# Performance work log

Measured on AMD Instinct MI355X. Metric: run time of the kernel, lower is better.

## Reference

```python
import jax, jax.numpy as jnp
import numpy as np

VOCAB, NUM_CLASSES, C, H = 50257, 1000, 32, 512
B, T = 64, 1024
DECAY = 0.85


def setup_inputs() -> dict:
    key = jax.random.key(0)
    ks = jax.random.split(key, 16)
    s = 0.02
    return {
        "tokens": jax.random.randint(ks[0], (B, T), 0, VOCAB, dtype=jnp.int32),
        "emb": jax.random.normal(ks[1], (VOCAB, H), jnp.float32) * s,
        "w_ih": jax.random.normal(ks[2], (3 * H, H), jnp.float32) * s,
        "w_hh": jax.random.normal(ks[3], (3 * H, H), jnp.float32) * s,
        "b_ih": jax.random.normal(ks[4], (3 * H,), jnp.float32) * s,
        "b_hh": jax.random.normal(ks[5], (3 * H,), jnp.float32) * s,
        "wc": jax.random.normal(ks[6], (C * H, H), jnp.float32) * s,
        "bc": jax.random.normal(ks[7], (C * H,), jnp.float32) * s,
        "ws": jax.random.normal(ks[8], (C, H), jnp.float32) * s,
        "bs": jax.random.normal(ks[9], (C,), jnp.float32) * s,
        "ww": jax.random.normal(ks[10], (C, H), jnp.float32) * s,
        "bw": jax.random.normal(ks[11], (C,), jnp.float32) * s,
        "wcls": jax.random.normal(ks[12], (NUM_CLASSES, C * (H + 2)), jnp.float32) * s,
        "bcls": jax.random.normal(ks[13], (NUM_CLASSES,), jnp.float32) * s,
    }


def _gru(x, w_ih, w_hh, b_ih, b_hh):
    # x: [B,T,H]; torch GRU gate order: r, z, n
    xp = jnp.einsum('bth,gh->btg', x, w_ih) + b_ih          # [B,T,3H], batched GEMM
    xp = jnp.transpose(xp, (1, 0, 2))                        # [T,B,3H]

    def step(h, xp_t):
        hp = h @ w_hh.T + b_hh                               # [B,3H]
        xr, xz, xn = jnp.split(xp_t, 3, axis=-1)
        hr, hz, hn = jnp.split(hp, 3, axis=-1)
        r = jax.nn.sigmoid(xr + hr)
        z = jax.nn.sigmoid(xz + hz)
        n = jnp.tanh(xn + r * hn)
        h_new = (1.0 - z) * n + z * h
        return h_new, h_new

    h0 = jnp.zeros((x.shape[0], w_hh.shape[1]), x.dtype)
    _, h_seq = jax.lax.scan(step, h0, xp)                    # [T,B,H]
    return h_seq


def reference(tokens, emb, w_ih, w_hh, b_ih, b_hh, wc, bc, ws, bs, ww, bw, wcls, bcls):
    x = emb[tokens]                                          # [B,T,H]
    h_seq = _gru(x, w_ih, w_hh, b_ih, b_hh)                  # [T,B,H]
    Tn = h_seq.shape[0]

    # EMA with constant decay d: state_T = d^T*init + (1-d) * sum_t d^(T-1-t) * delta_t
    decay = DECAY ** (Tn - 1 - jnp.arange(Tn, dtype=jnp.float32))  # [T]

    # centers (linear delta, init 0): project the decay-weighted hidden sum once.
    hw = jnp.einsum('t,tbh->bh', decay, h_seq)               # [B,H]
    centers = (1 - DECAY) * (hw @ wc.T + decay.sum() * bc)   # [B,C*H]
    centers = centers.reshape(-1, C, H)                      # [B,C,H]

    # spreads (sigmoid delta, init 1)
    sd = jax.nn.sigmoid(jnp.einsum('tbh,ch->tbc', h_seq, ws) + bs)  # [T,B,C]
    spreads = DECAY ** Tn + (1 - DECAY) * jnp.einsum('t,tbc->bc', decay, sd)

    # weights (plain additive accumulation)
    weights = h_seq.sum(axis=0) @ ww.T + Tn * bw             # [B,C]
    nw = jax.nn.softmax(weights, axis=-1)

    summary = jnp.concatenate(
        [centers, spreads[..., None], nw[..., None]], axis=-1)  # [B,C,H+2]
    flat = summary.reshape(summary.shape[0], -1)
    return flat @ wcls.T + bcls
```

## Files before the change

### kernel.cpp

```cpp
#include <hip/hip_runtime.h>
#include <stddef.h>


typedef unsigned short u16;
typedef short s8v __attribute__((ext_vector_type(8)));
typedef float f4v __attribute__((ext_vector_type(4)));

#define B_ 64
#define T_ 1024
#define H_ 512
#define G_ 1536
#define C_ 32
#define NCLS_ 1000
#define KCLS_ 16448

#define AGENT __HIP_MEMORY_SCOPE_AGENT

__device__ __forceinline__ u16 f2bf(float f) {
    unsigned u = __float_as_uint(f);
    unsigned r = (u + 0x7fffu + ((u >> 16) & 1u)) >> 16;
    return (u16)r;
}
__device__ __forceinline__ float b2f(u16 x) { return __uint_as_float(((unsigned)x) << 16); }
__device__ __forceinline__ float bflo(unsigned u) { return __uint_as_float(u << 16); }
__device__ __forceinline__ float bfhi(unsigned u) { return __uint_as_float(u & 0xffff0000u); }
__device__ __forceinline__ float sigmoidf_(float x) { return 1.0f / (1.0f + __expf(-x)); }
__device__ __forceinline__ float tanhf_(float x) { return 1.0f - 2.0f / (1.0f + __expf(2.0f * x)); }

__global__ void k_cast_wih(const float* __restrict__ src, u16* __restrict__ dst) {
    int i = blockIdx.x * 256 + threadIdx.x;
    if (i < G_ * H_) dst[i] = f2bf(src[i]);
}

__global__ void k_pack_whhN(const float* __restrict__ w_hh, uint4* __restrict__ wN) {
    int idx = blockIdx.x * 256 + threadIdx.x;
    if (idx >= 4 * 64 * 384) return;
    int g = idx % 384;
    int k8 = (idx / 384) % 64;
    int s = idx / (384 * 64);
    int j = (g >> 7) * 512 + s * 128 + (g & 127);
    const float* wr = w_hh + (size_t)j * H_ + 8 * k8;
    uint4 v;
    v.x = (unsigned)f2bf(wr[0]) | ((unsigned)f2bf(wr[1]) << 16);
    v.y = (unsigned)f2bf(wr[2]) | ((unsigned)f2bf(wr[3]) << 16);
    v.z = (unsigned)f2bf(wr[4]) | ((unsigned)f2bf(wr[5]) << 16);
    v.w = (unsigned)f2bf(wr[6]) | ((unsigned)f2bf(wr[7]) << 16);
    wN[idx] = v;
}

__global__ void k_decay(float* __restrict__ decay) {
    int t = blockIdx.x * 256 + threadIdx.x;
    if (t < T_) decay[t] = powf(0.85f, (float)(T_ - 1 - t));
}

__global__ void k_zero(float* __restrict__ p, int n) {
    int i = blockIdx.x * 256 + threadIdx.x;
    if (i < n) p[i] = 0.f;
}

__global__ __launch_bounds__(256) void k_embed(const int* __restrict__ tokens,
                                               const float* __restrict__ emb,
                                               u16* __restrict__ X) {
    int g = blockIdx.x * 256 + threadIdx.x;
    int m = g >> 6, c8 = g & 63;
    int tok = tokens[m];
    const float4* src = (const float4*)(emb + (size_t)tok * H_ + c8 * 8);
    float4 f0 = src[0], f1 = src[1];
    uint4 pk;
    pk.x = (unsigned)f2bf(f0.x) | ((unsigned)f2bf(f0.y) << 16);
    pk.y = (unsigned)f2bf(f0.z) | ((unsigned)f2bf(f0.w) << 16);
    pk.z = (unsigned)f2bf(f1.x) | ((unsigned)f2bf(f1.y) << 16);
    pk.w = (unsigned)f2bf(f1.z) | ((unsigned)f2bf(f1.w) << 16);
    *(uint4*)(X + (size_t)m * H_ + c8 * 8) = pk;
}

__global__ __launch_bounds__(256) void k_xp(const u16* __restrict__ X,
                                            const u16* __restrict__ Wih,
                                            const float* __restrict__ b_ih,
                                            u16* __restrict__ xp) {
    __shared__ u16 Bs[128 * 48];
    int tid = threadIdx.x;
    int bid = blockIdx.x;
    int m0 = (bid / 12) * 64;
    int n0 = (bid % 12) * 128;
    int w = tid >> 6, lane = tid & 63;
    int lm = lane & 15, q = lane >> 4;
    f4v acc[8];
#pragma unroll
    for (int i = 0; i < 8; i++) acc[i] = (f4v){0.f, 0.f, 0.f, 0.f};
    int arow = m0 + w * 16 + lm;
    const u16* Aptr = X + (size_t)arow * H_ + q * 8;
    int srow = tid >> 1, shalf = tid & 1;
    for (int kk = 0; kk < H_; kk += 32) {
        const uint4* src = (const uint4*)(Wih + (size_t)(n0 + srow) * H_ + kk + shalf * 16);
        uint4 v0 = src[0], v1 = src[1];
        uint4* dst = (uint4*)(Bs + srow * 48 + shalf * 16);
        dst[0] = v0; dst[1] = v1;
        __syncthreads();
        s8v a = *(const s8v*)(Aptr + kk);
#pragma unroll
        for (int nt = 0; nt < 8; nt++) {
            s8v bf = *(const s8v*)(Bs + (nt * 16 + lm) * 48 + q * 8);
            acc[nt] = __builtin_amdgcn_mfma_f32_16x16x32_bf16(a, bf, acc[nt], 0, 0, 0);
        }
        __syncthreads();
    }
#pragma unroll
    for (int nt = 0; nt < 8; nt++) {
        int col = n0 + nt * 16 + lm;
        float bias = b_ih[col];
#pragma unroll
        for (int r = 0; r < 4; r++) {
            int row = m0 + w * 16 + q * 4 + r;
            xp[(size_t)row * G_ + col] = f2bf(acc[nt][r] + bias);
        }
    }
}

__global__ __launch_bounds__(512, 2) void k_scan4(const uint4* __restrict__ wN,
                                                  const u16* __restrict__ xp,
                                                  const float* __restrict__ b_hh,
                                                  float* __restrict__ hseq,
                                                  float* __restrict__ hx,
                                                  unsigned* __restrict__ flags) {
    int x = blockIdx.x;
    int s = x & 3, b = x >> 2;
    int tid = threadIdx.x;
    __shared__ float hl[2][512];
    __shared__ float dotb[3][128];
    hl[0][tid] = 0.f;
    const uint4* wS = wN + (size_t)s * (64 * 384);
    int io = tid & 127;
    int jo = s * 128 + io;
    float bh = 0.f;
    if (tid < 384) bh = b_hh[(tid >> 7) * H_ + jo];
    float hprev = 0.f;
    const u16* xpb = xp + (size_t)b * T_ * G_;
    unsigned* flg = flags + b * 64;
    __syncthreads();
    for (int t = 0; t < T_; t++) {
        int par = t & 1;
        float xr = 0.f, xz = 0.f, xn = 0.f;
        if (tid < 128) {
            const u16* xt = xpb + (size_t)t * G_;
            xr = b2f(xt[jo]); xz = b2f(xt[512 + jo]); xn = b2f(xt[1024 + jo]);
        }
        float acc = 0.f;
        if (tid < 384) {
            const float4* h4 = (const float4*)&hl[par][s * 128];
            const uint4* wp = wS + (size_t)(16 * s) * 384 + tid;
#pragma unroll
            for (int kk = 0; kk < 16; kk++) {
                uint4 wv = wp[(size_t)kk * 384];
                float4 ha = h4[2 * kk], hb = h4[2 * kk + 1];
                acc = fmaf(bflo(wv.x), ha.x, acc); acc = fmaf(bfhi(wv.x), ha.y, acc);
                acc = fmaf(bflo(wv.y), ha.z, acc); acc = fmaf(bfhi(wv.y), ha.w, acc);
                acc = fmaf(bflo(wv.z), hb.x, acc); acc = fmaf(bfhi(wv.z), hb.y, acc);
                acc = fmaf(bflo(wv.w), hb.z, acc); acc = fmaf(bfhi(wv.w), hb.w, acc);
            }
        } else if (t > 0) {
            int p = tid - 384;
            const float* hr = hx + ((size_t)par * B_ + b) * 512;
#pragma unroll
            for (int d = 1; d < 4; d++) {
                int s2 = (s + d) & 3;
                const unsigned* fl = flg + s2 * 16;
                while (__hip_atomic_load(fl, __ATOMIC_RELAXED, AGENT) < (unsigned)t)
                    __builtin_amdgcn_s_sleep(1);
                __asm__ __volatile__("" ::: "memory");
                hl[par][s2 * 128 + p] =
                    __hip_atomic_load(hr + s2 * 128 + p, __ATOMIC_RELAXED, AGENT);
            }
        }
        __syncthreads();
        if (tid < 384) {
#pragma unroll
            for (int d = 1; d < 4; d++) {
                int s2 = (s + d) & 3;
                const float4* h4 = (const float4*)&hl[par][s2 * 128];
                const uint4* wp = wS + (size_t)(16 * s2) * 384 + tid;
#pragma unroll
                for (int kk = 0; kk < 16; kk++) {
                    uint4 wv = wp[(size_t)kk * 384];
                    float4 ha = h4[2 * kk], hb = h4[2 * kk + 1];
                    acc = fmaf(bflo(wv.x), ha.x, acc); acc = fmaf(bfhi(wv.x), ha.y, acc);
                    acc = fmaf(bflo(wv.y), ha.z, acc); acc = fmaf(bfhi(wv.y), ha.w, acc);
                    acc = fmaf(bflo(wv.z), hb.x, acc); acc = fmaf(bfhi(wv.z), hb.y, acc);
                    acc = fmaf(bflo(wv.w), hb.z, acc); acc = fmaf(bfhi(wv.w), hb.w, acc);
                }
            }
            dotb[tid >> 7][io] = acc + bh;
        }
        __syncthreads();
        if (tid < 128) {
            float r = sigmoidf_(xr + dotb[0][io]);
            float z = sigmoidf_(xz + dotb[1][io]);
            float n = tanhf_(xn + r * dotb[2][io]);
            float hn = (1.f - z) * n + z * hprev;
            hprev = hn;
            hl[par ^ 1][jo] = hn;
            __hip_atomic_store(hx + ((size_t)(par ^ 1) * B_ + b) * 512 + jo, hn,
                               __ATOMIC_RELAXED, AGENT);
            hseq[((size_t)t * B_ + b) * H_ + jo] = hn;
        }
        __syncthreads();
        if (tid == 0)
            __hip_atomic_store(flg + s * 16, (unsigned)(t + 1), __ATOMIC_RELAXED, AGENT);
    }
}

__global__ __launch_bounds__(512) void k_hw8(const float* __restrict__ hseq,
                                             const float* __restrict__ decay,
                                             float* __restrict__ hwT,
                                             float* __restrict__ hsumT) {
    int b = blockIdx.x & 63, chunk = blockIdx.x >> 6;
    int h = threadIdx.x;
    int t0 = chunk * 128;
    float aw = 0.f, as = 0.f;
    for (int tt = 0; tt < 128; tt++) {
        float v = hseq[((size_t)(t0 + tt) * B_ + b) * H_ + h];
        aw = fmaf(decay[t0 + tt], v, aw);
        as += v;
    }
    atomicAdd(&hwT[h * B_ + b], aw);
    atomicAdd(&hsumT[h * B_ + b], as);
}

__global__ __launch_bounds__(512) void k_sd8(const float* __restrict__ hseq,
                                             const float* __restrict__ ws,
                                             const float* __restrict__ bs,
                                             const float* __restrict__ decay,
                                             float* __restrict__ flatT) {
    int b = blockIdx.x & 63, chunk = blockIdx.x >> 6;
    int t0 = chunk * 128;
    int tid = threadIdx.x;
    __shared__ float hl[2][512];
    int c = tid >> 4, p = tid & 15;
    float wreg[32];
#pragma unroll
    for (int i = 0; i < 32; i++) wreg[i] = ws[c * H_ + p + 16 * i];
    float bsc = bs[c];
    float acc = 0.f;
    hl[0][tid] = hseq[((size_t)t0 * B_ + b) * H_ + tid];
    __syncthreads();
    for (int tt = 0; tt < 128; tt++) {
        float nxt = 0.f;
        if (tt < 127) nxt = hseq[((size_t)(t0 + tt + 1) * B_ + b) * H_ + tid];
        int pg = tt & 1;
        float partial = 0.f;
#pragma unroll
        for (int i = 0; i < 32; i++) partial = fmaf(wreg[i], hl[pg][p + 16 * i], partial);
        partial += __shfl_xor(partial, 1, 16);
        partial += __shfl_xor(partial, 2, 16);
        partial += __shfl_xor(partial, 4, 16);
        partial += __shfl_xor(partial, 8, 16);
        acc = fmaf(decay[t0 + tt], sigmoidf_(partial + bsc), acc);
        __syncthreads();
        hl[pg ^ 1][tid] = nxt;
        __syncthreads();
    }
    if (p == 0) atomicAdd(&flatT[(c * 514 + 512) * B_ + b], 0.15f * acc);
}

__global__ __launch_bounds__(1024) void k_weights(const float* __restrict__ hsumT,
                                                  const float* __restrict__ ww,
                                                  const float* __restrict__ bw,
                                                  float* __restrict__ flatT) {
    int tid = threadIdx.x;
    __shared__ float wmat[C_ * B_];
    __shared__ float mb[B_], sb[B_];
    int b = tid & 63;
    int c0 = tid >> 6;
    float a0 = 0.f, a1 = 0.f;
    for (int h = 0; h < H_; h++) {
        float hv = hsumT[h * B_ + b];
        a0 = fmaf(ww[c0 * H_ + h], hv, a0);
        a1 = fmaf(ww[(c0 + 16) * H_ + h], hv, a1);
    }
    wmat[c0 * B_ + b] = a0 + 1024.0f * bw[c0];
    wmat[(c0 + 16) * B_ + b] = a1 + 1024.0f * bw[c0 + 16];
    __syncthreads();
    if (tid < 64) {
        float m = -1e30f;
        for (int c = 0; c < C_; c++) m = fmaxf(m, wmat[c * B_ + tid]);
        float sum = 0.f;
        for (int c = 0; c < C_; c++) sum += __expf(wmat[c * B_ + tid] - m);
        mb[tid] = m;
        sb[tid] = 1.0f / sum;
    }
    __syncthreads();
    flatT[(c0 * 514 + 513) * B_ + b] = __expf(wmat[c0 * B_ + b] - mb[b]) * sb[b];
    flatT[((c0 + 16) * 514 + 513) * B_ + b] = __expf(wmat[(c0 + 16) * B_ + b] - mb[b]) * sb[b];
}

__global__ __launch_bounds__(64) void k_centersT(const float* __restrict__ hwT,
                                                 const float* __restrict__ wc,
                                                 const float* __restrict__ bc,
                                                 float* __restrict__ flatT) {
    int b = threadIdx.x;
    int k0 = blockIdx.x * 8;
    float acc[8] = {0, 0, 0, 0, 0, 0, 0, 0};
    for (int h = 0; h < H_; h++) {
        float hv = hwT[h * B_ + b];
#pragma unroll
        for (int r = 0; r < 8; r++) acc[r] = fmaf(wc[(size_t)(k0 + r) * H_ + h], hv, acc[r]);
    }
#pragma unroll
    for (int r = 0; r < 8; r++) {
        int k = k0 + r;
        int c = k >> 9, i = k & 511;
        flatT[(c * 514 + i) * B_ + b] = 0.15f * (acc[r] + (1.0f / 0.15f) * bc[k]);
    }
}

__global__ __launch_bounds__(256) void k_cls(const float* __restrict__ flatT,
                                             const float* __restrict__ wcls,
                                             const float* __restrict__ bcls,
                                             float* __restrict__ out) {
    int tid = threadIdx.x;
    int wv = tid >> 6, b = tid & 63;
    int j0 = blockIdx.x * 8;
    __shared__ float red[4][8][64];
    float acc[8] = {0, 0, 0, 0, 0, 0, 0, 0};
    for (int i = 0; i < 4112; i++) {
        int k = wv * 4112 + i;
        float fv = flatT[k * B_ + b];
#pragma unroll
        for (int r = 0; r < 8; r++) acc[r] = fmaf(wcls[(size_t)(j0 + r) * KCLS_ + k], fv, acc[r]);
    }
#pragma unroll
    for (int r = 0; r < 8; r++) red[wv][r][b] = acc[r];
    __syncthreads();
    for (int rr = tid; rr < 512; rr += 256) {
        int r = rr >> 6, bb = rr & 63;
        float sum = red[0][r][bb] + red[1][r][bb] + red[2][r][bb] + red[3][r][bb];
        out[bb * NCLS_ + j0 + r] = sum + bcls[j0 + r];
    }
}

extern "C" void kernel_launch(void* const* d_in, const int* in_sizes, int n_in,
                              void* d_out, int out_size, void* d_ws, size_t ws_size,
                              hipStream_t stream) {
    const int*   tokens = (const int*)d_in[0];
    const float* emb    = (const float*)d_in[1];
    const float* w_ih   = (const float*)d_in[2];
    const float* w_hh   = (const float*)d_in[3];
    const float* b_ih   = (const float*)d_in[4];
    const float* b_hh   = (const float*)d_in[5];
    const float* wc     = (const float*)d_in[6];
    const float* bc     = (const float*)d_in[7];
    const float* ws     = (const float*)d_in[8];
    const float* bs     = (const float*)d_in[9];
    const float* ww     = (const float*)d_in[10];
    const float* bw     = (const float*)d_in[11];
    const float* wcls   = (const float*)d_in[12];
    const float* bcls   = (const float*)d_in[13];
    float* out = (float*)d_out;

    char* w = (char*)d_ws;
    u16*      xp    = (u16*)(w + 0);
    float*    hseq  = (float*)(w + 201326592);
    u16*      X16   = (u16*)(w + 335544320);
    u16*      Wih16 = (u16*)(w + 402653184);
    uint4*    wN    = (uint4*)(w + 404226048);
    float*    decay = (float*)(w + 405798912);
    float*    hwT   = (float*)(w + 405803008);
    float*    hsumT = (float*)(w + 405934080);
    float*    flatT = (float*)(w + 406065152);
    float*    hx    = (float*)(w + 335544320);
    unsigned* flags = (unsigned*)(w + 335544320 + 262144);

    k_cast_wih<<<dim3((G_ * H_ + 255) / 256), dim3(256), 0, stream>>>(w_ih, Wih16);
    k_pack_whhN<<<dim3((4 * 64 * 384 + 255) / 256), dim3(256), 0, stream>>>(w_hh, wN);
    k_decay<<<dim3(4), dim3(256), 0, stream>>>(decay);
    k_zero<<<dim3((1118208 + 255) / 256), dim3(256), 0, stream>>>(hwT, 1118208);
    k_embed<<<dim3(16384), dim3(256), 0, stream>>>(tokens, emb, X16);
    k_xp<<<dim3(12288), dim3(256), 0, stream>>>(X16, Wih16, b_ih, xp);
    k_zero<<<dim3(16), dim3(256), 0, stream>>>((float*)flags, 4096);
    k_scan4<<<dim3(256), dim3(512), 0, stream>>>(wN, xp, b_hh, hseq, hx, flags);
    k_hw8<<<dim3(512), dim3(512), 0, stream>>>(hseq, decay, hwT, hsumT);
    k_sd8<<<dim3(512), dim3(512), 0, stream>>>(hseq, ws, bs, decay, flatT);
    k_weights<<<dim3(1), dim3(1024), 0, stream>>>(hsumT, ww, bw, flatT);
    k_centersT<<<dim3(2048), dim3(64), 0, stream>>>(hwT, wc, bc, flatT);
    k_cls<<<dim3(125), dim3(256), 0, stream>>>(flatT, wcls, bcls, out);
}
```

Measured before the change: 11.47 ms.

## Rewrite GRU recurrence as MFMA matmul across 16 blocks with bf16 hidden exchange

The recurrent scan now partitions the hidden dimension across 16 blocks. Each block computes all 64 batch rows with bf16 MFMA instructions, keeping the W_hh r/z tiles in registers and the n tile in LDS. This replaces the per-batch 4-way split that used scalar FMA dot products. The hidden state is exchanged through global memory as packed bf16, with per-wave flags polled by a whole wave at once. The goal is to shorten each sequential step and the number of synchronisations. The cost is heavy register pressure, bf16 rounding of h, and cross-block polling across all 16 blocks.

```diff
diff --git a/kernel.cpp b/kernel.cpp
--- a/kernel.cpp
+++ b/kernel.cpp
@@ -3,6 +3,7 @@
 
 
 typedef unsigned short u16;
+typedef unsigned long long u64t;
 typedef short s8v __attribute__((ext_vector_type(8)));
 typedef float f4v __attribute__((ext_vector_type(4)));
 
@@ -15,6 +16,7 @@
 #define KCLS_ 16448
 
 #define AGENT __HIP_MEMORY_SCOPE_AGENT
+#define MFMA16(a, b, c) __builtin_amdgcn_mfma_f32_16x16x32_bf16(a, b, c, 0, 0, 0)
 
 __device__ __forceinline__ u16 f2bf(float f) {
     unsigned u = __float_as_uint(f);
@@ -27,25 +29,38 @@
 __device__ __forceinline__ float sigmoidf_(float x) { return 1.0f / (1.0f + __expf(-x)); }
 __device__ __forceinline__ float tanhf_(float x) { return 1.0f - 2.0f / (1.0f + __expf(2.0f * x)); }
 
+__device__ __forceinline__ s8v pull16(const u16* p) {
+    union { u64t u[2]; s8v v; } x;
+    x.u[0] = __hip_atomic_load((const u64t*)p, __ATOMIC_RELAXED, AGENT);
+    x.u[1] = __hip_atomic_load((const u64t*)(p + 4), __ATOMIC_RELAXED, AGENT);
+    return x.v;
+}
+
 __global__ void k_cast_wih(const float* __restrict__ src, u16* __restrict__ dst) {
     int i = blockIdx.x * 256 + threadIdx.x;
     if (i < G_ * H_) dst[i] = f2bf(src[i]);
 }
 
-__global__ void k_pack_whhN(const float* __restrict__ w_hh, uint4* __restrict__ wN) {
+__global__ void k_packA(const float* __restrict__ w_hh, uint4* __restrict__ Apk) {
     int idx = blockIdx.x * 256 + threadIdx.x;
-    if (idx >= 4 * 64 * 384) return;
-    int g = idx % 384;
-    int k8 = (idx / 384) % 64;
-    int s = idx / (384 * 64);
-    int j = (g >> 7) * 512 + s * 128 + (g & 127);
-    const float* wr = w_hh + (size_t)j * H_ + 8 * k8;
+    if (idx >= 98304) return;
+    int lane = idx & 63;
+    int kstep = (idx >> 6) & 15;
+    int g10 = idx >> 10;
+    int gate = g10 % 3;
+    int bi = g10 / 3;
+    int ih = bi & 1;
+    int blk = bi >> 1;
+    int lm = lane & 15, q = lane >> 4;
+    int row = gate * 512 + blk * 32 + ih * 16 + lm;
+    int k0 = kstep * 32 + q * 8;
+    const float* wr = w_hh + (size_t)row * H_ + k0;
     uint4 v;
     v.x = (unsigned)f2bf(wr[0]) | ((unsigned)f2bf(wr[1]) << 16);
     v.y = (unsigned)f2bf(wr[2]) | ((unsigned)f2bf(wr[3]) << 16);
     v.z = (unsigned)f2bf(wr[4]) | ((unsigned)f2bf(wr[5]) << 16);
     v.w = (unsigned)f2bf(wr[6]) | ((unsigned)f2bf(wr[7]) << 16);
-    wN[idx] = v;
+    Apk[idx] = v;
 }
 
 __global__ void k_decay(float* __restrict__ decay) {
@@ -101,7 +116,7 @@
 #pragma unroll
         for (int nt = 0; nt < 8; nt++) {
             s8v bf = *(const s8v*)(Bs + (nt * 16 + lm) * 48 + q * 8);
-            acc[nt] = __builtin_amdgcn_mfma_f32_16x16x32_bf16(a, bf, acc[nt], 0, 0, 0);
+            acc[nt] = MFMA16(a, bf, acc[nt]);
         }
         __syncthreads();
     }
@@ -117,95 +132,119 @@
     }
 }
 
-__global__ __launch_bounds__(512, 2) void k_scan4(const uint4* __restrict__ wN,
-                                                  const u16* __restrict__ xp,
-                                                  const float* __restrict__ b_hh,
-                                                  float* __restrict__ hseq,
-                                                  float* __restrict__ hx,
-                                                  unsigned* __restrict__ flags) {
-    int x = blockIdx.x;
-    int s = x & 3, b = x >> 2;
+__global__ __launch_bounds__(512, 2) void k_scan_mfma(const uint4* __restrict__ Apk,
+                                                      const u16* __restrict__ xp,
+                                                      const float* __restrict__ b_hh,
+                                                      float* __restrict__ hseq,
+                                                      u16* __restrict__ hx,
+                                                      unsigned* __restrict__ flags) {
+    int blk = blockIdx.x;
     int tid = threadIdx.x;
-    __shared__ float hl[2][512];
-    __shared__ float dotb[3][128];
-    hl[0][tid] = 0.f;
-    const uint4* wS = wN + (size_t)s * (64 * 384);
-    int io = tid & 127;
-    int jo = s * 128 + io;
-    float bh = 0.f;
-    if (tid < 384) bh = b_hh[(tid >> 7) * H_ + jo];
-    float hprev = 0.f;
-    const u16* xpb = xp + (size_t)b * T_ * G_;
-    unsigned* flg = flags + b * 64;
+    int w = tid >> 6, lane = tid & 63;
+    int btile = w >> 1, ihalf = w & 1;
+    int q = lane >> 4, lm = lane & 15;
+    int i0 = blk * 32;
+    int b = btile * 16 + lm;
+    int ibase = i0 + ihalf * 16 + q * 4;
+
+    __shared__ uint4 AnL[2 * 16 * 64];
+    for (int r = tid; r < 2048; r += 512) {
+        int ih = r >> 10, rest = r & 1023;
+        AnL[r] = Apk[(size_t)((blk * 2 + ih) * 3 + 2) * 1024 + rest];
+    }
+
+    const uint4* apb = Apk + (size_t)(blk * 2 + ihalf) * 3 * 1024;
+    s8v Ar[16], Az[16];
+#pragma unroll
+    for (int k = 0; k < 16; k++) Ar[k] = *(const s8v*)(apb + k * 64 + lane);
+#pragma unroll
+    for (int k = 0; k < 16; k++) Az[k] = *(const s8v*)(apb + 1024 + k * 64 + lane);
+
+    float bhr[4], bhz[4], bhn[4];
+#pragma unroll
+    for (int j = 0; j < 4; j++) {
+        bhr[j] = b_hh[ibase + j];
+        bhz[j] = b_hh[512 + ibase + j];
+        bhn[j] = b_hh[1024 + ibase + j];
+    }
+
+    const u16* xpb = xp + (size_t)b * T_ * G_ + ibase;
+    uint2 xR = *(const uint2*)(xpb);
+    uint2 xZ = *(const uint2*)(xpb + 512);
+    uint2 xN = *(const uint2*)(xpb + 1024);
+
+    const unsigned* fpoll = flags + btile * 32;
+    unsigned* fself = flags + btile * 32 + blk * 2 + ihalf;
+
+    float hprev[4] = {0.f, 0.f, 0.f, 0.f};
     __syncthreads();
-    for (int t = 0; t < T_; t++) {
+
+#pragma unroll 1
+    for (int t = 0; t < T_; ++t) {
         int par = t & 1;
-        float xr = 0.f, xz = 0.f, xn = 0.f;
-        if (tid < 128) {
-            const u16* xt = xpb + (size_t)t * G_;
-            xr = b2f(xt[jo]); xz = b2f(xt[512 + jo]); xn = b2f(xt[1024 + jo]);
-        }
-        float acc = 0.f;
-        if (tid < 384) {
-            const float4* h4 = (const float4*)&hl[par][s * 128];
-            const uint4* wp = wS + (size_t)(16 * s) * 384 + tid;
-#pragma unroll
-            for (int kk = 0; kk < 16; kk++) {
-                uint4 wv = wp[(size_t)kk * 384];
-                float4 ha = h4[2 * kk], hb = h4[2 * kk + 1];
-                acc = fmaf(bflo(wv.x), ha.x, acc); acc = fmaf(bfhi(wv.x), ha.y, acc);
-                acc = fmaf(bflo(wv.y), ha.z, acc); acc = fmaf(bfhi(wv.y), ha.w, acc);
-                acc = fmaf(bflo(wv.z), hb.x, acc); acc = fmaf(bfhi(wv.z), hb.y, acc);
-                acc = fmaf(bflo(wv.w), hb.z, acc); acc = fmaf(bfhi(wv.w), hb.w, acc);
+        if (t) {
+            while (1) {
+                unsigned f = (lane < 32)
+                                 ? __hip_atomic_load(fpoll + lane, __ATOMIC_RELAXED, AGENT)
+                                 : 0xffffffffu;
+                if (__all((int)(f >= (unsigned)t))) break;
+                __builtin_amdgcn_s_sleep(1);
             }
-        } else if (t > 0) {
-            int p = tid - 384;
-            const float* hr = hx + ((size_t)par * B_ + b) * 512;
-#pragma unroll
-            for (int d = 1; d < 4; d++) {
-                int s2 = (s + d) & 3;
-                const unsigned* fl = flg + s2 * 16;
-                while (__hip_atomic_load(fl, __ATOMIC_RELAXED, AGENT) < (unsigned)t)
-                    __builtin_amdgcn_s_sleep(1);
-                __asm__ __volatile__("" ::: "memory");
-                hl[par][s2 * 128 + p] =
-                    __hip_atomic_load(hr + s2 * 128 + p, __ATOMIC_RELAXED, AGENT);
-            }
-        }
-        __syncthreads();
-        if (tid < 384) {
-#pragma unroll
-            for (int d = 1; d < 4; d++) {
-                int s2 = (s + d) & 3;
-                const float4* h4 = (const float4*)&hl[par][s2 * 128];
-                const uint4* wp = wS + (size_t)(16 * s2) * 384 + tid;
-#pragma unroll
-                for (int kk = 0; kk < 16; kk++) {
-                    uint4 wv = wp[(size_t)kk * 384];
-                    float4 ha = h4[2 * kk], hb = h4[2 * kk + 1];
-                    acc = fmaf(bflo(wv.x), ha.x, acc); acc = fmaf(bfhi(wv.x), ha.y, acc);
-                    acc = fmaf(bflo(wv.y), ha.z, acc); acc = fmaf(bfhi(wv.y), ha.w, acc);
-                    acc = fmaf(bflo(wv.z), hb.x, acc); acc = fmaf(bfhi(wv.z), hb.y, acc);
-                    acc = fmaf(bflo(wv.w), hb.z, acc); acc = fmaf(bfhi(wv.w), hb.w, acc);
-                }
-            }
-            dotb[tid >> 7][io] = acc + bh;
-        }
-        __syncthreads();
-        if (tid < 128) {
-            float r = sigmoidf_(xr + dotb[0][io]);
-            float z = sigmoidf_(xz + dotb[1][io]);
-            float n = tanhf_(xn + r * dotb[2][io]);
-            float hn = (1.f - z) * n + z * hprev;
-            hprev = hn;
-            hl[par ^ 1][jo] = hn;
-            __hip_atomic_store(hx + ((size_t)(par ^ 1) * B_ + b) * 512 + jo, hn,
-                               __ATOMIC_RELAXED, AGENT);
-            hseq[((size_t)t * B_ + b) * H_ + jo] = hn;
-        }
-        __syncthreads();
-        if (tid == 0)
-            __hip_atomic_store(flg + s * 16, (unsigned)(t + 1), __ATOMIC_RELAXED, AGENT);
+            __asm__ __volatile__("" ::: "memory");
+        }
+
+        const u16* hb = hx + par * 32768 + b * 512 + q * 8;
+        f4v aR = {0.f, 0.f, 0.f, 0.f};
+        f4v aZ = {0.f, 0.f, 0.f, 0.f};
+        f4v aN = {0.f, 0.f, 0.f, 0.f};
+        s8v hfp[8];
+#pragma unroll
+        for (int k = 0; k < 8; k++) hfp[k] = pull16(hb + k * 32);
+#pragma unroll
+        for (int k = 0; k < 8; k++) {
+            s8v an = *(const s8v*)(AnL + (ihalf * 16 + k) * 64 + lane);
+            aR = MFMA16(Ar[k], hfp[k], aR);
+            aZ = MFMA16(Az[k], hfp[k], aZ);
+            aN = MFMA16(an, hfp[k], aN);
+            hfp[k] = pull16(hb + (k + 8) * 32);
+        }
+#pragma unroll
+        for (int k = 0; k < 8; k++) {
+            s8v an = *(const s8v*)(AnL + (ihalf * 16 + 8 + k) * 64 + lane);
+            aR = MFMA16(Ar[k + 8], hfp[k], aR);
+            aZ = MFMA16(Az[k + 8], hfp[k], aZ);
+            aN = MFMA16(an, hfp[k], aN);
+        }
+
+        float xr[4] = {bflo(xR.x), bfhi(xR.x), bflo(xR.y), bfhi(xR.y)};
+        float xz[4] = {bflo(xZ.x), bfhi(xZ.x), bflo(xZ.y), bfhi(xZ.y)};
+        float xn[4] = {bflo(xN.x), bfhi(xN.x), bflo(xN.y), bfhi(xN.y)};
+        float hnew[4];
+#pragma unroll
+        for (int j = 0; j < 4; j++) {
+            float rg = sigmoidf_(xr[j] + aR[j] + bhr[j]);
+            float zg = sigmoidf_(xz[j] + aZ[j] + bhz[j]);
+            float ng = tanhf_(xn[j] + rg * (aN[j] + bhn[j]));
+            hnew[j] = (1.f - zg) * ng + zg * hprev[j];
+            hprev[j] = hnew[j];
+        }
+
+        u64t pk = (u64t)f2bf(hnew[0]) | ((u64t)f2bf(hnew[1]) << 16) |
+                  ((u64t)f2bf(hnew[2]) << 32) | ((u64t)f2bf(hnew[3]) << 48);
+        __hip_atomic_store((u64t*)(hx + (par ^ 1) * 32768 + b * 512 + ibase), pk,
+                           __ATOMIC_RELAXED, AGENT);
+        __asm__ __volatile__("s_waitcnt vmcnt(0)" ::: "memory");
+        if (lane == 0)
+            __hip_atomic_store(fself, (unsigned)(t + 1), __ATOMIC_RELAXED, AGENT);
+
+        f4v hv = {hnew[0], hnew[1], hnew[2], hnew[3]};
+        *(f4v*)(hseq + ((size_t)t * B_ + b) * H_ + ibase) = hv;
+
+        int tn = (t + 1 < T_) ? t + 1 : t;
+        const u16* xpt = xpb + (size_t)tn * G_;
+        xR = *(const uint2*)(xpt);
+        xZ = *(const uint2*)(xpt + 512);
+        xN = *(const uint2*)(xpt + 1024);
     }
 }
 
@@ -362,22 +401,22 @@
     float*    hseq  = (float*)(w + 201326592);
     u16*      X16   = (u16*)(w + 335544320);
     u16*      Wih16 = (u16*)(w + 402653184);
-    uint4*    wN    = (uint4*)(w + 404226048);
+    uint4*    Apk   = (uint4*)(w + 404226048);
     float*    decay = (float*)(w + 405798912);
     float*    hwT   = (float*)(w + 405803008);
     float*    hsumT = (float*)(w + 405934080);
     float*    flatT = (float*)(w + 406065152);
-    float*    hx    = (float*)(w + 335544320);
-    unsigned* flags = (unsigned*)(w + 335544320 + 262144);
+    u16*      hx    = (u16*)(w + 335544320);
+    unsigned* flags = (unsigned*)(w + 335544320 + 131072);
 
     k_cast_wih<<<dim3((G_ * H_ + 255) / 256), dim3(256), 0, stream>>>(w_ih, Wih16);
-    k_pack_whhN<<<dim3((4 * 64 * 384 + 255) / 256), dim3(256), 0, stream>>>(w_hh, wN);
+    k_packA<<<dim3(384), dim3(256), 0, stream>>>(w_hh, Apk);
     k_decay<<<dim3(4), dim3(256), 0, stream>>>(decay);
     k_zero<<<dim3((1118208 + 255) / 256), dim3(256), 0, stream>>>(hwT, 1118208);
     k_embed<<<dim3(16384), dim3(256), 0, stream>>>(tokens, emb, X16);
     k_xp<<<dim3(12288), dim3(256), 0, stream>>>(X16, Wih16, b_ih, xp);
-    k_zero<<<dim3(16), dim3(256), 0, stream>>>((float*)flags, 4096);
-    k_scan4<<<dim3(256), dim3(512), 0, stream>>>(wN, xp, b_hh, hseq, hx, flags);
+    k_zero<<<dim3(129), dim3(256), 0, stream>>>((float*)hx, 32896);
+    k_scan_mfma<<<dim3(16), dim3(512), 0, stream>>>(Apk, xp, b_hh, hseq, hx, flags);
     k_hw8<<<dim3(512), dim3(512), 0, stream>>>(hseq, decay, hwT, hsumT);
     k_sd8<<<dim3(512), dim3(512), 0, stream>>>(hseq, ws, bs, decay, flatT);
     k_weights<<<dim3(1), dim3(1024), 0, stream>>>(hsumT, ww, bw, flatT);
```

Result: slower. 12.18 ms (+6.2%).
